# Kernel optimization log

Measured on AMD Instinct MI355X. Metric: run time of the kernel, lower is better.

## Reference

```python
import jax, jax.numpy as jnp
import numpy as np

N, H, E, R, Q = 10000, 128, 160000, 32, 1
CUT = 5.0  # cutoff_upper, cutoff_lower = 0


def setup_inputs() -> dict:
    key = jax.random.key(0)
    ks = jax.random.split(key, 16)

    def w(k, shape, fan_in):
        return jax.random.normal(k, shape, jnp.float32) / np.sqrt(fan_in).astype(np.float32)

    return dict(
        X=jax.random.normal(ks[0], (N, H, 3, 3), jnp.float32),
        charges=jax.random.normal(ks[1], (N, Q), jnp.float32),
        edge_attr=jax.random.normal(ks[2], (E, R), jnp.float32),
        edge_weight=jax.random.uniform(ks[3], (E,), jnp.float32, 0.0, CUT),
        W1=w(ks[4], (H, R + 2 * Q), R + 2 * Q), b1=jnp.zeros((H,), jnp.float32),
        W2=w(ks[5], (2 * H, H), H), b2=jnp.zeros((2 * H,), jnp.float32),
        W3=w(ks[6], (3 * H, 2 * H), 2 * H), b3=jnp.zeros((3 * H,), jnp.float32),
        Wt0=w(ks[7], (H, H), H), Wt1=w(ks[8], (H, H), H), Wt2=w(ks[9], (H, H), H),
        Wt3=w(ks[10], (H, H), H), Wt4=w(ks[11], (H, H), H), Wt5=w(ks[12], (H, H), H),
        edge_index=jax.random.randint(ks[13], (2, E), 0, N),
    )


def tensor_norm(T):
    return jnp.sum(T * T, axis=(-2, -1))  # [N, H]


def decompose(T):
    # I: mean of diagonal (scalar per channel); A: skew part; S: traceless symmetric part
    I = jnp.trace(T, axis1=-2, axis2=-1) / 3.0  # [N, H]
    Tt = jnp.swapaxes(T, -2, -1)
    A = 0.5 * (T - Tt)
    S = 0.5 * (T + Tt) - I[..., None, None] * jnp.eye(3, dtype=T.dtype)
    return I, A, S


def chlin(T, W):
    # channel-mixing linear on [N, H, 3, 3]; torch Linear: y_o = sum_h x_h W[o, h]
    return jnp.einsum('nhij,oh->noij', T, W)


def vec_to_skew(v):
    # v: [N, H, 3] -> skew-symmetric [N, H, 3, 3]
    z = jnp.zeros_like(v[..., 0])
    return jnp.stack([
        jnp.stack([z, -v[..., 2], v[..., 1]], -1),
        jnp.stack([v[..., 2], z, -v[..., 0]], -1),
        jnp.stack([-v[..., 1], v[..., 0], z], -1),
    ], -2)


def skew_to_vec(A):
    return jnp.stack([A[..., 2, 1], A[..., 0, 2], A[..., 1, 0]], -1)


def reference(X, charges, edge_attr, edge_weight, W1, b1, W2, b2, W3, b3,
              Wt0, Wt1, Wt2, Wt3, Wt4, Wt5, edge_index):
    eye = jnp.eye(3, dtype=X.dtype)
    src, dst = edge_index[0], edge_index[1]
    n = X.shape[0]

    # cosine cutoff (cutoff_lower = 0)
    C = 0.5 * (jnp.cos(jnp.pi * edge_weight / CUT) + 1.0) * (edge_weight < CUT)

    # edge scalar MLP
    x = jnp.concatenate([edge_attr, charges[src], charges[dst]], axis=-1)
    x = jax.nn.silu(x @ W1.T + b1)
    x = jax.nn.silu(x @ W2.T + b2)
    x = jax.nn.silu(x @ W3.T + b3)
    x = (x * C[:, None]).reshape(-1, 3, H)  # [E, 3, H]

    X = X / (tensor_norm(X) + 1.0)[..., None, None]
    I, A, S = decompose(X)
    I = I @ Wt0.T
    A = chlin(A, Wt1)
    S = chlin(S, Wt2)
    Y = A + S + I[..., None, None] * eye

    # message passing: gather at dst, weight by edge scalars, scatter-add to src
    Im = jax.ops.segment_sum(x[:, 0, :] * I[dst], src, num_segments=n)
    Am = jax.ops.segment_sum(x[:, 1, :, None] * skew_to_vec(A)[dst], src, num_segments=n)
    Sm = jax.ops.segment_sum(x[:, 2, :, None, None] * S[dst], src, num_segments=n)
    msg = vec_to_skew(Am) + Sm + Im[..., None, None] * eye

    # O(3) equivariance: symmetrized product
    M = jnp.matmul(msg, Y) + jnp.matmul(Y, msg)
    I, A, S = decompose(M)

    _X = A + S + I[..., None, None] * eye
    normp1 = tensor_norm(_X) + 1.0
    I = I / normp1
    A = A / normp1[..., None, None]
    S = S / normp1[..., None, None]
    I = I @ Wt3.T
    A = chlin(A, Wt4)
    S = chlin(S, Wt5)
    dX = A + S + I[..., None, None] * eye
    return X + dX + jnp.matmul(dX, dX)
```

## Files before the change

### kernel.cpp

```cpp
#include <hip/hip_runtime.h>

#define NN  10000
#define HD  128
#define EE  160000
#define RD  32
#define NH  (NN * HD)

typedef __attribute__((ext_vector_type(8))) short short8_t;
typedef __attribute__((ext_vector_type(4))) float f32x4_t;
typedef __attribute__((ext_vector_type(4))) int   int4_t;

__device__ __forceinline__ float silu_f(float z) {
    return z * __builtin_amdgcn_rcpf(1.0f + __expf(-z));
}
__device__ __forceinline__ short f2b(float v) {
    unsigned u = __float_as_uint(v);
    unsigned r = (u + 0x7FFFu + ((u >> 16) & 1u)) >> 16;
    return (short)r;
}
__device__ __forceinline__ float b2f(short s) {
    return __uint_as_float(((unsigned)(unsigned short)s) << 16);
}
__device__ __forceinline__ unsigned cvt_pk(float a, float b) {
    unsigned r;
    asm("v_cvt_pk_bf16_f32 %0, %1, %2" : "=v"(r) : "v"(a), "v"(b));
    return r;
}

__global__ __launch_bounds__(256) void k_wconv(
    const float* __restrict__ W1, const float* __restrict__ W2,
    const float* __restrict__ W3,
    const float* __restrict__ Wt0, const float* __restrict__ Wt1,
    const float* __restrict__ Wt2, const float* __restrict__ Wt3,
    const float* __restrict__ Wt4, const float* __restrict__ Wt5,
    short* __restrict__ W1b, short* __restrict__ W2b, short* __restrict__ W3b,
    short* __restrict__ WtPh, short* __restrict__ WtPl,
    short* __restrict__ WtFh, short* __restrict__ WtFl)
{
    const int i = blockIdx.x * 256 + threadIdx.x;
    if (i < 8192) {
        const int j = i & 7, lane = (i >> 3) & 63;
        const int kb = (i >> 9) & 1, ct = i >> 10;
        const int n = ct * 16 + (lane & 15);
        const int k = kb * 32 + (lane >> 4) * 8 + j;
        W1b[i] = (k < 34) ? f2b(W1[n * 34 + k]) : (short)0;
        return;
    }
    int j2 = i - 8192;
    if (j2 < 32768) {
        const int j = j2 & 7, lane = (j2 >> 3) & 63;
        const int kb = (j2 >> 9) & 3, ct = j2 >> 11;
        const int n = ct * 16 + (lane & 15);
        const int k = kb * 32 + (lane >> 4) * 8 + j;
        W2b[j2] = f2b(W2[n * 128 + k]);
        return;
    }
    j2 -= 32768;
    if (j2 < 98304) {
        const int j = j2 & 7, lane = (j2 >> 3) & 63;
        const int kb = (j2 >> 9) & 7, ct = j2 >> 12;
        const int n = ct * 16 + (lane & 15);
        const int k = kb * 32 + (lane >> 4) * 8 + j;
        W3b[j2] = f2b(W3[n * 256 + k]);
        return;
    }
    j2 -= 98304;
    if (j2 < 6 * 16384) {
        const int m = j2 >> 14, idx = j2 & 16383;
        const float* src = (m == 0) ? Wt0 : (m == 1) ? Wt1 : (m == 2) ? Wt2
                         : (m == 3) ? Wt3 : (m == 4) ? Wt4 : Wt5;
        const float w = src[idx];
        const short hi = f2b(w);
        const short lo = f2b(w - b2f(hi));
        if (m < 3) { WtPh[m * 16384 + idx] = hi; WtPl[m * 16384 + idx] = lo; }
        else       { WtFh[(m - 3) * 16384 + idx] = hi; WtFl[(m - 3) * 16384 + idx] = lo; }
    }
}

template <bool FIN, bool WB>
__global__ __launch_bounds__(512, 4) void k_mix(
    const float* __restrict__ X,
    const float* __restrict__ Yin, const float* __restrict__ MSGin,
    const short* __restrict__ Wh,  const short* __restrict__ Wl,
    float* __restrict__ outp, short* __restrict__ ybf)
{
    extern __shared__ __align__(16) char smem[];
    short* sBh = (short*)smem;
    short* sBl = sBh + 144 * 128;
    float* sC  = (float*)smem;

    const int tid = threadIdx.x;
    const int n0  = blockIdx.x * 16;

#pragma unroll 2
    for (int i = 0; i < 4; i++) {
        const int p  = i * 512 + tid;
        const int nl = p >> 7, h = p & 127;
        float dec[9];
        if constexpr (!FIN) {
            const float* t = X + ((size_t)((n0 + nl) * HD + h)) * 9;
            float T[9];
#pragma unroll
            for (int q = 0; q < 9; q++) T[q] = t[q];
            float nrm = 0.f;
#pragma unroll
            for (int q = 0; q < 9; q++) nrm = fmaf(T[q], T[q], nrm);
            const float inv = 1.0f / (nrm + 1.0f);
#pragma unroll
            for (int q = 0; q < 9; q++) T[q] *= inv;
            const float I = (T[0] + T[4] + T[8]) * (1.0f / 3.0f);
            dec[0] = I;
            dec[1] = 0.5f * (T[7] - T[5]);
            dec[2] = 0.5f * (T[2] - T[6]);
            dec[3] = 0.5f * (T[3] - T[1]);
            dec[4] = T[0] - I;
            dec[5] = 0.5f * (T[1] + T[3]);
            dec[6] = 0.5f * (T[2] + T[6]);
            dec[7] = T[4] - I;
            dec[8] = 0.5f * (T[5] + T[7]);
        } else {
            const int basep = (n0 + nl) * HD + h;
            float yv[9], mv[9];
#pragma unroll
            for (int c = 0; c < 9; c++) {
                yv[c] = Yin[(size_t)c * NH + basep];
                mv[c] = MSGin[(size_t)c * NH + basep];
            }
            float Yt[9], G[9];
            {
                const float I = yv[0], a0 = yv[1], a1 = yv[2], a2 = yv[3];
                const float s00 = yv[4], s01 = yv[5], s02 = yv[6], s11 = yv[7], s12 = yv[8];
                const float s22 = -s00 - s11;
                Yt[0] = I + s00; Yt[1] = s01 - a2; Yt[2] = s02 + a1;
                Yt[3] = s01 + a2; Yt[4] = I + s11; Yt[5] = s12 - a0;
                Yt[6] = s02 - a1; Yt[7] = s12 + a0; Yt[8] = I + s22;
            }
            {
                const float I = mv[0], a0 = mv[1], a1 = mv[2], a2 = mv[3];
                const float s00 = mv[4], s01 = mv[5], s02 = mv[6], s11 = mv[7], s12 = mv[8];
                const float s22 = -s00 - s11;
                G[0] = I + s00; G[1] = s01 - a2; G[2] = s02 + a1;
                G[3] = s01 + a2; G[4] = I + s11; G[5] = s12 - a0;
                G[6] = s02 - a1; G[7] = s12 + a0; G[8] = I + s22;
            }
            float M[9];
#pragma unroll
            for (int r = 0; r < 3; r++)
#pragma unroll
                for (int cc = 0; cc < 3; cc++) {
                    float a = 0.f;
#pragma unroll
                    for (int k = 0; k < 3; k++)
                        a += G[r * 3 + k] * Yt[k * 3 + cc]
                           + Yt[r * 3 + k] * G[k * 3 + cc];
                    M[r * 3 + cc] = a;
                }
            const float I2 = (M[0] + M[4] + M[8]) * (1.0f / 3.0f);
            const float a0 = 0.5f * (M[7] - M[5]);
            const float a1 = 0.5f * (M[2] - M[6]);
            const float a2 = 0.5f * (M[3] - M[1]);
            const float s00 = M[0] - I2, s11 = M[4] - I2;
            const float s01 = 0.5f * (M[1] + M[3]);
            const float s02 = 0.5f * (M[2] + M[6]);
            const float s12 = 0.5f * (M[5] + M[7]);
            const float s22 = -s00 - s11;
            const float nrm = 2.f * (a0 * a0 + a1 * a1 + a2 * a2)
                            + (s00 * s00 + s11 * s11 + s22 * s22)
                            + 2.f * (s01 * s01 + s02 * s02 + s12 * s12)
                            + 3.f * I2 * I2;
            const float inv = 1.0f / (nrm + 1.0f);
            dec[0] = I2 * inv;  dec[1] = a0 * inv;  dec[2] = a1 * inv;
            dec[3] = a2 * inv;  dec[4] = s00 * inv; dec[5] = s01 * inv;
            dec[6] = s02 * inv; dec[7] = s11 * inv; dec[8] = s12 * inv;
        }
        const int sw = (nl & 7) << 3;
        const int hx = h ^ sw;
#pragma unroll
        for (int c = 0; c < 9; c++) {
            const float v  = dec[c];
            const short hi = f2b(v);
            const short lo = f2b(v - b2f(hi));
            const int idx = (c * 16 + nl) * 128 + hx;
            sBh[idx] = hi;
            sBl[idx] = lo;
        }
    }
    __syncthreads();

    const int lane = tid & 63, wid = tid >> 6;
    const int l15 = lane & 15, g = lane >> 4;
    f32x4_t acc[9];
#pragma unroll
    for (int c = 0; c < 9; c++) acc[c] = {0.f, 0.f, 0.f, 0.f};

    const int bsw = (l15 & 7) << 3;
    const int o   = wid * 16 + l15;
#pragma unroll
    for (int k = 0; k < 4; k++) {
        const int k0  = k * 32 + g * 8;
        const int ksw = k0 ^ bsw;
#pragma unroll
        for (int w = 0; w < 3; w++) {
            const size_t aoff = (size_t)w * 16384 + (size_t)o * 128 + k0;
            const short8_t Ah = *(const short8_t*)(Wh + aoff);
            const short8_t Al = *(const short8_t*)(Wl + aoff);
            const int ct0 = (w == 0) ? 0 : (w == 1 ? 1 : 4);
            const int ctn = (w == 0) ? 1 : (w == 1 ? 3 : 5);
            for (int cc = 0; cc < ctn; cc++) {
                const int ct = ct0 + cc;
                const int boff = (ct * 16 + l15) * 128 + ksw;
                const short8_t Bh = *(const short8_t*)&sBh[boff];
                const short8_t Bl = *(const short8_t*)&sBl[boff];
                acc[ct] = __builtin_amdgcn_mfma_f32_16x16x32_bf16(Al, Bh, acc[ct], 0, 0, 0);
                acc[ct] = __builtin_amdgcn_mfma_f32_16x16x32_bf16(Ah, Bl, acc[ct], 0, 0, 0);
                acc[ct] = __builtin_amdgcn_mfma_f32_16x16x32_bf16(Ah, Bh, acc[ct], 0, 0, 0);
            }
        }
    }
    __syncthreads();

    const int csw = (l15 & 7) << 2;
    {
        const int o0 = wid * 16 + g * 4;
#pragma unroll
        for (int ct = 0; ct < 9; ct++)
            *(f32x4_t*)&sC[(ct * 16 + l15) * 128 + (o0 ^ csw)] = acc[ct];
    }
    __syncthreads();

    if constexpr (!FIN) {
        for (int i = tid; i < 144 * 32; i += 512) {
            const int row = i >> 5, q = i & 31;
            const int c = row >> 4, nl = row & 15;
            const int sw = (nl & 7) << 2;
            const f32x4_t v = *(const f32x4_t*)&sC[row * 128 + ((q * 4) ^ sw)];
            const size_t oo = (size_t)c * NH + (size_t)(n0 + nl) * HD + q * 4;
            *(f32x4_t*)&outp[oo] = v;
            if constexpr (WB) {
                uint2 u;
                u.x = cvt_pk(v[0], v[1]);
                u.y = cvt_pk(v[2], v[3]);
                *(uint2*)&ybf[oo] = u;
            }
        }
    } else {
#pragma unroll 2
        for (int i = 0; i < 4; i++) {
            const int p  = i * 512 + tid;
            const int nl = p >> 7, oo = p & 127;
            const int sw = (nl & 7) << 2;
            const int ox = oo ^ sw;
            float a9[9];
#pragma unroll
            for (int c = 0; c < 9; c++) a9[c] = sC[(c * 16 + nl) * 128 + ox];
            float D[9];
            {
                const float I = a9[0], a0 = a9[1], a1 = a9[2], a2 = a9[3];
                const float s00 = a9[4], s01 = a9[5], s02 = a9[6];
                const float s11 = a9[7], s12 = a9[8];
                const float s22 = -s00 - s11;
                D[0] = I + s00; D[1] = s01 - a2; D[2] = s02 + a1;
                D[3] = s01 + a2; D[4] = I + s11; D[5] = s12 - a0;
                D[6] = s02 - a1; D[7] = s12 + a0; D[8] = I + s22;
            }
            const size_t xbase = ((size_t)((n0 + nl) * HD + oo)) * 9;
            float T[9];
#pragma unroll
            for (int q = 0; q < 9; q++) T[q] = X[xbase + q];
            float nrm = 0.f;
#pragma unroll
            for (int q = 0; q < 9; q++) nrm = fmaf(T[q], T[q], nrm);
            const float inv = 1.0f / (nrm + 1.0f);
            float* op = outp + xbase;
#pragma unroll
            for (int r = 0; r < 3; r++)
#pragma unroll
                for (int cc = 0; cc < 3; cc++) {
                    float dd2 = 0.f;
#pragma unroll
                    for (int k = 0; k < 3; k++)
                        dd2 = fmaf(D[r * 3 + k], D[k * 3 + cc], dd2);
                    op[r * 3 + cc] = T[r * 3 + cc] * inv + D[r * 3 + cc] + dd2;
                }
        }
    }
}

__global__ __launch_bounds__(256) void k_count(const int* __restrict__ EI,
                                               int* __restrict__ cnt)
{
    const int e = blockIdx.x * 256 + threadIdx.x;
    atomicAdd(&cnt[EI[e]], 1);
}

__global__ __launch_bounds__(256) void k_scan(const int* __restrict__ cnt,
                                              int* __restrict__ offs,
                                              int* __restrict__ cur)
{
    __shared__ int part[256];
    const int tid = threadIdx.x;
    const int per = (NN + 255) / 256;
    int s = 0;
    for (int i = 0; i < per; i++) {
        const int idx = tid * per + i;
        if (idx < NN) s += cnt[idx];
    }
    part[tid] = s;
    __syncthreads();
    if (tid == 0) {
        int r = 0;
        for (int i = 0; i < 256; i++) { const int t = part[i]; part[i] = r; r += t; }
        offs[NN] = r;
    }
    __syncthreads();
    int run = part[tid];
    for (int i = 0; i < per; i++) {
        const int idx = tid * per + i;
        if (idx < NN) {
            offs[idx] = run;
            cur[idx]  = run;
            run += cnt[idx];
        }
    }
}

__global__ __launch_bounds__(256) void k_fill(const int* __restrict__ EI,
                                              int* __restrict__ cur,
                                              int* __restrict__ EIDS,
                                              int* __restrict__ DSTS)
{
    const int e = blockIdx.x * 256 + threadIdx.x;
    const int s = EI[e];
    const int pos = atomicAdd(&cur[s], 1);
    EIDS[pos] = e;
    DSTS[pos] = EI[EE + e];
}

__global__ __launch_bounds__(512, 4) void k_edge_mfma(
    const float* __restrict__ EA, const float* __restrict__ CH,
    const float* __restrict__ EW, const int*   __restrict__ EI,
    const short* __restrict__ W1b, const float* __restrict__ b1,
    const short* __restrict__ W2b, const float* __restrict__ b2,
    const short* __restrict__ W3b, const float* __restrict__ b3,
    short* __restrict__ XC)
{
    __shared__ __align__(16) short sH2[64 * 256];
    __shared__ __align__(16) short sH1[64 * 128];
    __shared__ float sCut[64];

    short* sIn = sH2;
    const int tid = threadIdx.x;
    const int e0  = blockIdx.x * 64;

    {
        int4_t z = {0, 0, 0, 0};
        ((int4_t*)sIn)[tid] = z;
    }
    __syncthreads();
    {
        const float4 v = ((const float4*)(EA + (size_t)e0 * RD))[tid];
        const int e = tid >> 3;
        const int k = (tid & 7) * 4;
        short4 sv;
        sv.x = f2b(v.x); sv.y = f2b(v.y); sv.z = f2b(v.z); sv.w = f2b(v.w);
        *(short4*)&sIn[e * 64 + (k ^ ((e & 7) << 3))] = sv;
        if (tid < 64) {
            const int ee = tid;
            const int s = EI[e0 + ee];
            const int d = EI[EE + e0 + ee];
            const int sw = (ee & 7) << 3;
            sIn[ee * 64 + (32 ^ sw)] = f2b(CH[s]);
            sIn[ee * 64 + (33 ^ sw)] = f2b(CH[d]);
            const float w = EW[e0 + ee];
            sCut[ee] = (w < 5.0f)
                     ? 0.5f * (__cosf(0.62831853071795864769f * w) + 1.0f) : 0.0f;
        }
    }
    __syncthreads();

    const int lane = tid & 63;
    const int wid  = tid >> 6;
    const int l15  = lane & 15;
    const int g    = lane >> 4;
    const int fsw  = l15 << 3;

    {
        short8_t E1[4][2];
#pragma unroll
        for (int at = 0; at < 4; at++) {
            const int row = at * 16 + l15;
            const int x = (row & 7) << 3;
            E1[at][0] = *(const short8_t*)&sIn[row * 64 + ((g * 8) ^ x)];
            E1[at][1] = *(const short8_t*)&sIn[row * 64 + ((32 + g * 8) ^ x)];
        }
        const int ct = wid;
        const float4 b4 = *(const float4*)&b1[ct * 16 + g * 4];
        const short8_t av0 = *(const short8_t*)(W1b + (size_t)((ct * 2 + 0) * 64 + lane) * 8);
        const short8_t av1 = *(const short8_t*)(W1b + (size_t)((ct * 2 + 1) * 64 + lane) * 8);
        const int fcol = ct * 16 + g * 4;
#pragma unroll
        for (int at = 0; at < 4; at++) {
            f32x4_t acc = {b4.x, b4.y, b4.z, b4.w};
            acc = __builtin_amdgcn_mfma_f32_16x16x32_bf16(av0, E1[at][0], acc, 0, 0, 0);
            acc = __builtin_amdgcn_mfma_f32_16x16x32_bf16(av1, E1[at][1], acc, 0, 0, 0);
            const int edge = at * 16 + l15;
            uint2 u;
            u.x = cvt_pk(silu_f(acc[0]), silu_f(acc[1]));
            u.y = cvt_pk(silu_f(acc[2]), silu_f(acc[3]));
            *(uint2*)&sH1[edge * 128 + (fcol ^ fsw)] = u;
        }
    }
    __syncthreads();

    {
        short8_t E2[4][4];
#pragma unroll
        for (int at = 0; at < 4; at++) {
            const int row = at * 16 + l15;
            const int x = (row & 15) << 3;
#pragma unroll
            for (int kb = 0; kb < 4; kb++)
                E2[at][kb] = *(const short8_t*)&sH1[row * 128 + ((kb * 32 + g * 8) ^ x)];
        }
#pragma unroll
        for (int c = 0; c < 2; c++) {
            const int ct = c * 8 + wid;
            const float4 b4 = *(const float4*)&b2[ct * 16 + g * 4];
            const int fcol = ct * 16 + g * 4;
            f32x4_t acc[4];
#pragma unroll
            for (int at = 0; at < 4; at++) acc[at] = {b4.x, b4.y, b4.z, b4.w};
#pragma unroll
            for (int kb = 0; kb < 4; kb++) {
                const short8_t av = *(const short8_t*)(W2b + (size_t)((ct * 4 + kb) * 64 + lane) * 8);
#pragma unroll
                for (int at = 0; at < 4; at++)
                    acc[at] = __builtin_amdgcn_mfma_f32_16x16x32_bf16(av, E2[at][kb], acc[at], 0, 0, 0);
            }
#pragma unroll
            for (int at = 0; at < 4; at++) {
                const int edge = at * 16 + l15;
                uint2 u;
                u.x = cvt_pk(silu_f(acc[at][0]), silu_f(acc[at][1]));
                u.y = cvt_pk(silu_f(acc[at][2]), silu_f(acc[at][3]));
                *(uint2*)&sH2[edge * 256 + (fcol ^ fsw)] = u;
            }
        }
    }
    __syncthreads();

    {
        short8_t E3[4][8];
#pragma unroll
        for (int at = 0; at < 4; at++) {
            const int row = at * 16 + l15;
            const int x = (row & 15) << 3;
#pragma unroll
            for (int kb = 0; kb < 8; kb++)
                E3[at][kb] = *(const short8_t*)&sH2[row * 256 + ((kb * 32 + g * 8) ^ x)];
        }
        float cut[4];
#pragma unroll
        for (int at = 0; at < 4; at++) cut[at] = sCut[at * 16 + l15];
        for (int c = 0; c < 3; c++) {
            const int ct = c * 8 + wid;
            const float4 b4 = *(const float4*)&b3[ct * 16 + g * 4];
            const int fcol = ct * 16 + g * 4;
            f32x4_t acc[4];
#pragma unroll
            for (int at = 0; at < 4; at++) acc[at] = {b4.x, b4.y, b4.z, b4.w};
#pragma unroll
            for (int kb = 0; kb < 8; kb++) {
                const short8_t av = *(const short8_t*)(W3b + (size_t)((ct * 8 + kb) * 64 + lane) * 8);
#pragma unroll
                for (int at = 0; at < 4; at++)
                    acc[at] = __builtin_amdgcn_mfma_f32_16x16x32_bf16(av, E3[at][kb], acc[at], 0, 0, 0);
            }
#pragma unroll
            for (int at = 0; at < 4; at++) {
                const int edge = at * 16 + l15;
                const float cv = cut[at];
                uint2 u;
                u.x = cvt_pk(silu_f(acc[at][0]) * cv, silu_f(acc[at][1]) * cv);
                u.y = cvt_pk(silu_f(acc[at][2]) * cv, silu_f(acc[at][3]) * cv);
                *(uint2*)&XC[(size_t)(e0 + edge) * 384 + fcol] = u;
            }
        }
    }
}

__global__ __launch_bounds__(256) void k_edge_atomic(
    const float* __restrict__ EA, const float* __restrict__ CH,
    const float* __restrict__ EW, const int*   __restrict__ EI,
    const float* __restrict__ W1, const float* __restrict__ b1,
    const float* __restrict__ W2, const float* __restrict__ b2,
    const float* __restrict__ W3, const float* __restrict__ b3,
    const float* __restrict__ Y,  float* __restrict__ MSG)
{
    __shared__ __align__(16) float sInf[32 * 35];
    __shared__ __align__(16) float sH1f[32 * 132];
    __shared__ __align__(16) float sH2f[32 * 260];
    __shared__ __align__(16) float sXcf[32 * 132];
    __shared__ float sCc[32];
    __shared__ int   sS[32], sD[32];

    const int e0  = blockIdx.x * 32;
    const int tid = threadIdx.x;

    {
        const float4 v = ((const float4*)(EA + (size_t)e0 * RD))[tid];
        const int e = tid >> 3;
        const int k = (tid & 7) * 4;
        float* p = sInf + e * 35 + k;
        p[0] = v.x; p[1] = v.y; p[2] = v.z; p[3] = v.w;
    }
    if (tid < 32) {
        const int e = tid;
        const int s = EI[e0 + e];
        const int d = EI[EE + e0 + e];
        sS[e] = s; sD[e] = d;
        sInf[e * 35 + 32] = CH[s];
        sInf[e * 35 + 33] = CH[d];
        const float w = EW[e0 + e];
        sCc[e] = (w < 5.0f) ? 0.5f * (__cosf(0.62831853071795864769f * w) + 1.0f)
                            : 0.0f;
    }
    __syncthreads();

    const int e  = tid & 31;
    const int og = tid >> 5;

    {
        float acc[16];
#pragma unroll
        for (int j = 0; j < 16; j++) acc[j] = b1[og * 16 + j];
        for (int k = 0; k < 34; k++) {
            const float v = sInf[e * 35 + k];
#pragma unroll
            for (int j = 0; j < 16; j++)
                acc[j] = fmaf(v, W1[(og * 16 + j) * 34 + k], acc[j]);
        }
#pragma unroll
        for (int j = 0; j < 16; j++)
            sH1f[e * 132 + og * 16 + j] = silu_f(acc[j]);
    }
    __syncthreads();

    {
        float acc[32];
#pragma unroll
        for (int j = 0; j < 32; j++) acc[j] = b2[og * 32 + j];
        for (int hq = 0; hq < 32; hq++) {
            const float4 v = *(const float4*)&sH1f[e * 132 + hq * 4];
#pragma unroll
            for (int j = 0; j < 32; j++) {
                const float4 w =
                    *(const float4*)&W2[(size_t)(og * 32 + j) * 128 + hq * 4];
                acc[j] = fmaf(v.x, w.x, fmaf(v.y, w.y,
                         fmaf(v.z, w.z, fmaf(v.w, w.w, acc[j]))));
            }
        }
#pragma unroll
        for (int j = 0; j < 32; j++)
            sH2f[e * 260 + og * 32 + j] = silu_f(acc[j]);
    }
    __syncthreads();

    for (int c = 0; c < 3; c++) {
        {
            float acc[16];
#pragma unroll
            for (int j = 0; j < 16; j++) acc[j] = b3[c * 128 + og * 16 + j];
            for (int hq = 0; hq < 64; hq++) {
                const float4 v = *(const float4*)&sH2f[e * 260 + hq * 4];
#pragma unroll
                for (int j = 0; j < 16; j++) {
                    const float4 w = *(const float4*)
                        &W3[(size_t)(c * 128 + og * 16 + j) * 256 + hq * 4];
                    acc[j] = fmaf(v.x, w.x, fmaf(v.y, w.y,
                             fmaf(v.z, w.z, fmaf(v.w, w.w, acc[j]))));
                }
            }
            const float cc = sCc[e];
#pragma unroll
            for (int j = 0; j < 16; j++)
                sXcf[e * 132 + og * 16 + j] = silu_f(acc[j]) * cc;
        }
        __syncthreads();
        {
            const int h  = tid & 127;
            const int eh = tid >> 7;
#pragma unroll 4
            for (int i = 0; i < 16; i++) {
                const int ee = (eh << 4) | i;
                const int s = sS[ee], d = sD[ee];
                const float xv = sXcf[ee * 132 + h];
                const int sb = s * HD + h, db = d * HD + h;
                if (c == 0) {
                    atomicAdd(&MSG[0 * (size_t)NH + sb], xv * Y[0 * (size_t)NH + db]);
                } else if (c == 1) {
#pragma unroll
                    for (int cc2 = 1; cc2 < 4; cc2++)
                        atomicAdd(&MSG[(size_t)cc2 * NH + sb],
                                  xv * Y[(size_t)cc2 * NH + db]);
                } else {
#pragma unroll
                    for (int cc2 = 4; cc2 < 9; cc2++)
                        atomicAdd(&MSG[(size_t)cc2 * NH + sb],
                                  xv * Y[(size_t)cc2 * NH + db]);
                }
            }
        }
        __syncthreads();
    }
}

__device__ __forceinline__ float ldy(const float* p) { return *p; }
__device__ __forceinline__ float ldy(const short* p) { return b2f(*p); }

template <typename YT>
__global__ __launch_bounds__(256) void k_gather(
    const short* __restrict__ XC, const YT* __restrict__ Y,
    const int* __restrict__ offs, const int* __restrict__ EIDS,
    const int* __restrict__ DSTS, float* __restrict__ MSG)
{
    const int tid = threadIdx.x;
    const int nl  = tid >> 7, h = tid & 127;
    const int n   = blockIdx.x * 2 + nl;
    const int beg = offs[n], end = offs[n + 1];

    float m[9];
#pragma unroll
    for (int c = 0; c < 9; c++) m[c] = 0.f;

    for (int p = beg; p < end; ++p) {
        const int eid = EIDS[p];
        const int dst = DSTS[p];
        const size_t xb = (size_t)eid * 384;
        const float x0 = b2f(XC[xb + h]);
        const float x1 = b2f(XC[xb + 128 + h]);
        const float x2 = b2f(XC[xb + 256 + h]);
        const int yb = dst * HD + h;
        m[0] = fmaf(x0, ldy(Y + 0 * (size_t)NH + yb), m[0]);
        m[1] = fmaf(x1, ldy(Y + 1 * (size_t)NH + yb), m[1]);
        m[2] = fmaf(x1, ldy(Y + 2 * (size_t)NH + yb), m[2]);
        m[3] = fmaf(x1, ldy(Y + 3 * (size_t)NH + yb), m[3]);
        m[4] = fmaf(x2, ldy(Y + 4 * (size_t)NH + yb), m[4]);
        m[5] = fmaf(x2, ldy(Y + 5 * (size_t)NH + yb), m[5]);
        m[6] = fmaf(x2, ldy(Y + 6 * (size_t)NH + yb), m[6]);
        m[7] = fmaf(x2, ldy(Y + 7 * (size_t)NH + yb), m[7]);
        m[8] = fmaf(x2, ldy(Y + 8 * (size_t)NH + yb), m[8]);
    }
    const int base = n * HD + h;
#pragma unroll
    for (int c = 0; c < 9; c++) MSG[(size_t)c * NH + base] = m[c];
}

static inline size_t align_up(size_t v, size_t a) { return (v + a - 1) & ~(a - 1); }

extern "C" void kernel_launch(void* const* d_in, const int* in_sizes, int n_in,
                              void* d_out, int out_size, void* d_ws, size_t ws_size,
                              hipStream_t stream)
{
    const float* X   = (const float*)d_in[0];
    const float* CH  = (const float*)d_in[1];
    const float* EA  = (const float*)d_in[2];
    const float* EW  = (const float*)d_in[3];
    const float* W1  = (const float*)d_in[4];
    const float* b1  = (const float*)d_in[5];
    const float* W2  = (const float*)d_in[6];
    const float* b2  = (const float*)d_in[7];
    const float* W3  = (const float*)d_in[8];
    const float* b3  = (const float*)d_in[9];
    const float* Wt0 = (const float*)d_in[10];
    const float* Wt1 = (const float*)d_in[11];
    const float* Wt2 = (const float*)d_in[12];
    const float* Wt3 = (const float*)d_in[13];
    const float* Wt4 = (const float*)d_in[14];
    const float* Wt5 = (const float*)d_in[15];
    const int*   EI  = (const int*)d_in[16];
    float* out = (float*)d_out;

    size_t off = 0;
    float* Y    = (float*)((char*)d_ws + off); off = align_up(off + (size_t)9 * NH * 4, 64);
    float* MSG  = (float*)((char*)d_ws + off); off = align_up(off + (size_t)9 * NH * 4, 64);
    int*   cnt  = (int*)((char*)d_ws + off);   off = align_up(off + (size_t)NN * 4, 64);
    int*   cur  = (int*)((char*)d_ws + off);   off = align_up(off + (size_t)NN * 4, 64);
    int*   offs = (int*)((char*)d_ws + off);   off = align_up(off + (size_t)(NN + 1) * 4, 64);
    int*   EIDS = (int*)((char*)d_ws + off);   off = align_up(off + (size_t)EE * 4, 64);
    int*   DSTS = (int*)((char*)d_ws + off);   off = align_up(off + (size_t)EE * 4, 64);
    short* W1b  = (short*)((char*)d_ws + off); off = align_up(off + (size_t)8192 * 2, 64);
    short* W2b  = (short*)((char*)d_ws + off); off = align_up(off + (size_t)32768 * 2, 64);
    short* W3b  = (short*)((char*)d_ws + off); off = align_up(off + (size_t)98304 * 2, 64);
    short* WtPh = (short*)((char*)d_ws + off); off = align_up(off + (size_t)3 * 16384 * 2, 64);
    short* WtPl = (short*)((char*)d_ws + off); off = align_up(off + (size_t)3 * 16384 * 2, 64);
    short* WtFh = (short*)((char*)d_ws + off); off = align_up(off + (size_t)3 * 16384 * 2, 64);
    short* WtFl = (short*)((char*)d_ws + off); off = align_up(off + (size_t)3 * 16384 * 2, 64);
    short* XC   = (short*)((char*)d_ws + off); off = align_up(off + (size_t)EE * 384 * 2, 64);
    const size_t need_plain = off;
    short* Ybf  = (short*)((char*)d_ws + off); off = align_up(off + (size_t)9 * NH * 2, 64);
    const size_t need_ybf = off;

    k_wconv<<<928, 256, 0, stream>>>(W1, W2, W3, Wt0, Wt1, Wt2, Wt3, Wt4, Wt5,
                                     W1b, W2b, W3b, WtPh, WtPl, WtFh, WtFl);

    if (ws_size >= need_plain) {
        const bool use_ybf = (ws_size >= need_ybf);
        if (use_ybf)
            k_mix<false, true><<<NN / 16, 512, 73728, stream>>>(
                X, Y, Y, WtPh, WtPl, Y, Ybf);
        else
            k_mix<false, false><<<NN / 16, 512, 73728, stream>>>(
                X, Y, Y, WtPh, WtPl, Y, nullptr);

        hipMemsetAsync(cnt, 0, (size_t)NN * sizeof(int), stream);
        k_count<<<EE / 256, 256, 0, stream>>>(EI, cnt);
        k_scan<<<1, 256, 0, stream>>>(cnt, offs, cur);
        k_fill<<<EE / 256, 256, 0, stream>>>(EI, cur, EIDS, DSTS);
        k_edge_mfma<<<EE / 64, 512, 0, stream>>>(EA, CH, EW, EI,
                                                 W1b, b1, W2b, b2, W3b, b3, XC);
        if (use_ybf)
            k_gather<short><<<NN / 2, 256, 0, stream>>>(XC, Ybf, offs, EIDS, DSTS, MSG);
        else
            k_gather<float><<<NN / 2, 256, 0, stream>>>(XC, Y, offs, EIDS, DSTS, MSG);
    } else {
        k_mix<false, false><<<NN / 16, 512, 73728, stream>>>(
            X, Y, Y, WtPh, WtPl, Y, nullptr);
        hipMemsetAsync(MSG, 0, (size_t)9 * NH * sizeof(float), stream);
        k_edge_atomic<<<EE / 32, 256, 0, stream>>>(EA, CH, EW, EI,
                                                   W1, b1, W2, b2, W3, b3, Y, MSG);
    }

    k_mix<true, false><<<NN / 16, 512, 73728, stream>>>(X, Y, MSG, WtFh, WtFl, out, nullptr);
}
```

Measured before the change: 306.3 us.

## Fuse neighbor gather into final mix kernel and write edge filters in CSR order

The separate gather kernel is removed. The final mixing kernel now accumulates messages directly from CSR-ordered edge filters and the bf16 Y, so the fp32 MSG buffer no longer makes a global round trip. The edge MLP kernel reads edges through the sorted permutation (EIDS), so its XC output is stored in CSR order and the gather reads contiguous rows. The prep kernel also stops writing fp32 Y on the fast path. The trade-off is that the fused gather runs inside a 512-thread, high-LDS kernel with 16 nodes per block, which may reduce parallelism for the irregular gather loop. Reads of edge attributes inside the MLP kernel also become scattered.

```diff
diff --git a/kernel.cpp b/kernel.cpp
--- a/kernel.cpp
+++ b/kernel.cpp
@@ -77,12 +77,12 @@
     }
 }
 
-template <bool FIN, bool WB>
-__global__ __launch_bounds__(512, 4) void k_mix(
+
+template <bool YBF16>
+__global__ __launch_bounds__(512, 4) void k_mix_prep(
     const float* __restrict__ X,
-    const float* __restrict__ Yin, const float* __restrict__ MSGin,
-    const short* __restrict__ Wh,  const short* __restrict__ Wl,
-    float* __restrict__ outp, short* __restrict__ ybf)
+    const short* __restrict__ Wh, const short* __restrict__ Wl,
+    float* __restrict__ Yf, short* __restrict__ ybf)
 {
     extern __shared__ __align__(16) char smem[];
     short* sBh = (short*)smem;
@@ -96,83 +96,27 @@
     for (int i = 0; i < 4; i++) {
         const int p  = i * 512 + tid;
         const int nl = p >> 7, h = p & 127;
+        const float* t = X + ((size_t)((n0 + nl) * HD + h)) * 9;
+        float T[9];
+#pragma unroll
+        for (int q = 0; q < 9; q++) T[q] = t[q];
+        float nrm = 0.f;
+#pragma unroll
+        for (int q = 0; q < 9; q++) nrm = fmaf(T[q], T[q], nrm);
+        const float inv = 1.0f / (nrm + 1.0f);
+#pragma unroll
+        for (int q = 0; q < 9; q++) T[q] *= inv;
+        const float I = (T[0] + T[4] + T[8]) * (1.0f / 3.0f);
         float dec[9];
-        if constexpr (!FIN) {
-            const float* t = X + ((size_t)((n0 + nl) * HD + h)) * 9;
-            float T[9];
-#pragma unroll
-            for (int q = 0; q < 9; q++) T[q] = t[q];
-            float nrm = 0.f;
-#pragma unroll
-            for (int q = 0; q < 9; q++) nrm = fmaf(T[q], T[q], nrm);
-            const float inv = 1.0f / (nrm + 1.0f);
-#pragma unroll
-            for (int q = 0; q < 9; q++) T[q] *= inv;
-            const float I = (T[0] + T[4] + T[8]) * (1.0f / 3.0f);
-            dec[0] = I;
-            dec[1] = 0.5f * (T[7] - T[5]);
-            dec[2] = 0.5f * (T[2] - T[6]);
-            dec[3] = 0.5f * (T[3] - T[1]);
-            dec[4] = T[0] - I;
-            dec[5] = 0.5f * (T[1] + T[3]);
-            dec[6] = 0.5f * (T[2] + T[6]);
-            dec[7] = T[4] - I;
-            dec[8] = 0.5f * (T[5] + T[7]);
-        } else {
-            const int basep = (n0 + nl) * HD + h;
-            float yv[9], mv[9];
-#pragma unroll
-            for (int c = 0; c < 9; c++) {
-                yv[c] = Yin[(size_t)c * NH + basep];
-                mv[c] = MSGin[(size_t)c * NH + basep];
-            }
-            float Yt[9], G[9];
-            {
-                const float I = yv[0], a0 = yv[1], a1 = yv[2], a2 = yv[3];
-                const float s00 = yv[4], s01 = yv[5], s02 = yv[6], s11 = yv[7], s12 = yv[8];
-                const float s22 = -s00 - s11;
-                Yt[0] = I + s00; Yt[1] = s01 - a2; Yt[2] = s02 + a1;
-                Yt[3] = s01 + a2; Yt[4] = I + s11; Yt[5] = s12 - a0;
-                Yt[6] = s02 - a1; Yt[7] = s12 + a0; Yt[8] = I + s22;
-            }
-            {
-                const float I = mv[0], a0 = mv[1], a1 = mv[2], a2 = mv[3];
-                const float s00 = mv[4], s01 = mv[5], s02 = mv[6], s11 = mv[7], s12 = mv[8];
-                const float s22 = -s00 - s11;
-                G[0] = I + s00; G[1] = s01 - a2; G[2] = s02 + a1;
-                G[3] = s01 + a2; G[4] = I + s11; G[5] = s12 - a0;
-                G[6] = s02 - a1; G[7] = s12 + a0; G[8] = I + s22;
-            }
-            float M[9];
-#pragma unroll
-            for (int r = 0; r < 3; r++)
-#pragma unroll
-                for (int cc = 0; cc < 3; cc++) {
-                    float a = 0.f;
-#pragma unroll
-                    for (int k = 0; k < 3; k++)
-                        a += G[r * 3 + k] * Yt[k * 3 + cc]
-                           + Yt[r * 3 + k] * G[k * 3 + cc];
-                    M[r * 3 + cc] = a;
-                }
-            const float I2 = (M[0] + M[4] + M[8]) * (1.0f / 3.0f);
-            const float a0 = 0.5f * (M[7] - M[5]);
-            const float a1 = 0.5f * (M[2] - M[6]);
-            const float a2 = 0.5f * (M[3] - M[1]);
-            const float s00 = M[0] - I2, s11 = M[4] - I2;
-            const float s01 = 0.5f * (M[1] + M[3]);
-            const float s02 = 0.5f * (M[2] + M[6]);
-            const float s12 = 0.5f * (M[5] + M[7]);
-            const float s22 = -s00 - s11;
-            const float nrm = 2.f * (a0 * a0 + a1 * a1 + a2 * a2)
-                            + (s00 * s00 + s11 * s11 + s22 * s22)
-                            + 2.f * (s01 * s01 + s02 * s02 + s12 * s12)
-                            + 3.f * I2 * I2;
-            const float inv = 1.0f / (nrm + 1.0f);
-            dec[0] = I2 * inv;  dec[1] = a0 * inv;  dec[2] = a1 * inv;
-            dec[3] = a2 * inv;  dec[4] = s00 * inv; dec[5] = s01 * inv;
-            dec[6] = s02 * inv; dec[7] = s11 * inv; dec[8] = s12 * inv;
-        }
+        dec[0] = I;
+        dec[1] = 0.5f * (T[7] - T[5]);
+        dec[2] = 0.5f * (T[2] - T[6]);
+        dec[3] = 0.5f * (T[3] - T[1]);
+        dec[4] = T[0] - I;
+        dec[5] = 0.5f * (T[1] + T[3]);
+        dec[6] = 0.5f * (T[2] + T[6]);
+        dec[7] = T[4] - I;
+        dec[8] = 0.5f * (T[5] + T[7]);
         const int sw = (nl & 7) << 3;
         const int hx = h ^ sw;
 #pragma unroll
@@ -228,61 +172,217 @@
     }
     __syncthreads();
 
-    if constexpr (!FIN) {
-        for (int i = tid; i < 144 * 32; i += 512) {
-            const int row = i >> 5, q = i & 31;
-            const int c = row >> 4, nl = row & 15;
-            const int sw = (nl & 7) << 2;
-            const f32x4_t v = *(const f32x4_t*)&sC[row * 128 + ((q * 4) ^ sw)];
-            const size_t oo = (size_t)c * NH + (size_t)(n0 + nl) * HD + q * 4;
-            *(f32x4_t*)&outp[oo] = v;
-            if constexpr (WB) {
-                uint2 u;
-                u.x = cvt_pk(v[0], v[1]);
-                u.y = cvt_pk(v[2], v[3]);
-                *(uint2*)&ybf[oo] = u;
-            }
-        }
-    } else {
+    for (int i = tid; i < 144 * 32; i += 512) {
+        const int row = i >> 5, q = i & 31;
+        const int c = row >> 4, nl = row & 15;
+        const int sw = (nl & 7) << 2;
+        const f32x4_t v = *(const f32x4_t*)&sC[row * 128 + ((q * 4) ^ sw)];
+        const size_t oo = (size_t)c * NH + (size_t)(n0 + nl) * HD + q * 4;
+        if constexpr (YBF16) {
+            uint2 u;
+            u.x = cvt_pk(v[0], v[1]);
+            u.y = cvt_pk(v[2], v[3]);
+            *(uint2*)&ybf[oo] = u;
+        } else {
+            *(f32x4_t*)&Yf[oo] = v;
+        }
+    }
+}
+
+template <bool FUSED>
+__global__ __launch_bounds__(512, 4) void k_mix_fin(
+    const float* __restrict__ X,
+    const float* __restrict__ Yf,  const float* __restrict__ MSGf,
+    const short* __restrict__ Ybf, const short* __restrict__ XC,
+    const int* __restrict__ offs,  const int* __restrict__ DSTS,
+    const short* __restrict__ Wh,  const short* __restrict__ Wl,
+    float* __restrict__ outp)
+{
+    extern __shared__ __align__(16) char smem[];
+    short* sBh = (short*)smem;
+    short* sBl = sBh + 144 * 128;
+    float* sC  = (float*)smem;
+
+    const int tid = threadIdx.x;
+    const int n0  = blockIdx.x * 16;
+
+    for (int i = 0; i < 4; i++) {
+        const int p  = i * 512 + tid;
+        const int nl = p >> 7, h = p & 127;
+        const int basep = (n0 + nl) * HD + h;
+        float yv[9], mv[9];
+        if constexpr (FUSED) {
+            const int n = n0 + nl;
+            const int beg = offs[n], end = offs[n + 1];
+#pragma unroll
+            for (int c = 0; c < 9; c++) mv[c] = 0.f;
+            for (int pp = beg; pp < end; ++pp) {
+                const int dst = DSTS[pp];
+                const size_t xb = (size_t)pp * 384;
+                const float x0 = b2f(XC[xb + h]);
+                const float x1 = b2f(XC[xb + 128 + h]);
+                const float x2 = b2f(XC[xb + 256 + h]);
+                const int yb = dst * HD + h;
+                mv[0] = fmaf(x0, b2f(Ybf[0 * (size_t)NH + yb]), mv[0]);
+                mv[1] = fmaf(x1, b2f(Ybf[1 * (size_t)NH + yb]), mv[1]);
+                mv[2] = fmaf(x1, b2f(Ybf[2 * (size_t)NH + yb]), mv[2]);
+                mv[3] = fmaf(x1, b2f(Ybf[3 * (size_t)NH + yb]), mv[3]);
+                mv[4] = fmaf(x2, b2f(Ybf[4 * (size_t)NH + yb]), mv[4]);
+                mv[5] = fmaf(x2, b2f(Ybf[5 * (size_t)NH + yb]), mv[5]);
+                mv[6] = fmaf(x2, b2f(Ybf[6 * (size_t)NH + yb]), mv[6]);
+                mv[7] = fmaf(x2, b2f(Ybf[7 * (size_t)NH + yb]), mv[7]);
+                mv[8] = fmaf(x2, b2f(Ybf[8 * (size_t)NH + yb]), mv[8]);
+            }
+#pragma unroll
+            for (int c = 0; c < 9; c++) yv[c] = b2f(Ybf[(size_t)c * NH + basep]);
+        } else {
+#pragma unroll
+            for (int c = 0; c < 9; c++) {
+                yv[c] = Yf[(size_t)c * NH + basep];
+                mv[c] = MSGf[(size_t)c * NH + basep];
+            }
+        }
+        float Yt[9], G[9];
+        {
+            const float I = yv[0], a0 = yv[1], a1 = yv[2], a2 = yv[3];
+            const float s00 = yv[4], s01 = yv[5], s02 = yv[6], s11 = yv[7], s12 = yv[8];
+            const float s22 = -s00 - s11;
+            Yt[0] = I + s00; Yt[1] = s01 - a2; Yt[2] = s02 + a1;
+            Yt[3] = s01 + a2; Yt[4] = I + s11; Yt[5] = s12 - a0;
+            Yt[6] = s02 - a1; Yt[7] = s12 + a0; Yt[8] = I + s22;
+        }
+        {
+            const float I = mv[0], a0 = mv[1], a1 = mv[2], a2 = mv[3];
+            const float s00 = mv[4], s01 = mv[5], s02 = mv[6], s11 = mv[7], s12 = mv[8];
+            const float s22 = -s00 - s11;
+            G[0] = I + s00; G[1] = s01 - a2; G[2] = s02 + a1;
+            G[3] = s01 + a2; G[4] = I + s11; G[5] = s12 - a0;
+            G[6] = s02 - a1; G[7] = s12 + a0; G[8] = I + s22;
+        }
+        float M[9];
+#pragma unroll
+        for (int r = 0; r < 3; r++)
+#pragma unroll
+            for (int cc = 0; cc < 3; cc++) {
+                float a = 0.f;
+#pragma unroll
+                for (int k = 0; k < 3; k++)
+                    a += G[r * 3 + k] * Yt[k * 3 + cc]
+                       + Yt[r * 3 + k] * G[k * 3 + cc];
+                M[r * 3 + cc] = a;
+            }
+        const float I2 = (M[0] + M[4] + M[8]) * (1.0f / 3.0f);
+        const float a0 = 0.5f * (M[7] - M[5]);
+        const float a1 = 0.5f * (M[2] - M[6]);
+        const float a2 = 0.5f * (M[3] - M[1]);
+        const float s00 = M[0] - I2, s11 = M[4] - I2;
+        const float s01 = 0.5f * (M[1] + M[3]);
+        const float s02 = 0.5f * (M[2] + M[6]);
+        const float s12 = 0.5f * (M[5] + M[7]);
+        const float s22 = -s00 - s11;
+        const float nrm = 2.f * (a0 * a0 + a1 * a1 + a2 * a2)
+                        + (s00 * s00 + s11 * s11 + s22 * s22)
+                        + 2.f * (s01 * s01 + s02 * s02 + s12 * s12)
+                        + 3.f * I2 * I2;
+        const float inv = 1.0f / (nrm + 1.0f);
+        float dec[9];
+        dec[0] = I2 * inv;  dec[1] = a0 * inv;  dec[2] = a1 * inv;
+        dec[3] = a2 * inv;  dec[4] = s00 * inv; dec[5] = s01 * inv;
+        dec[6] = s02 * inv; dec[7] = s11 * inv; dec[8] = s12 * inv;
+
+        const int sw = (nl & 7) << 3;
+        const int hx = h ^ sw;
+#pragma unroll
+        for (int c = 0; c < 9; c++) {
+            const float v  = dec[c];
+            const short hi = f2b(v);
+            const short lo = f2b(v - b2f(hi));
+            const int idx = (c * 16 + nl) * 128 + hx;
+            sBh[idx] = hi;
+            sBl[idx] = lo;
+        }
+    }
+    __syncthreads();
+
+    const int lane = tid & 63, wid = tid >> 6;
+    const int l15 = lane & 15, g = lane >> 4;
+    f32x4_t acc[9];
+#pragma unroll
+    for (int c = 0; c < 9; c++) acc[c] = {0.f, 0.f, 0.f, 0.f};
+
+    const int bsw = (l15 & 7) << 3;
+    const int o   = wid * 16 + l15;
+#pragma unroll
+    for (int k = 0; k < 4; k++) {
+        const int k0  = k * 32 + g * 8;
+        const int ksw = k0 ^ bsw;
+#pragma unroll
+        for (int w = 0; w < 3; w++) {
+            const size_t aoff = (size_t)w * 16384 + (size_t)o * 128 + k0;
+            const short8_t Ah = *(const short8_t*)(Wh + aoff);
+            const short8_t Al = *(const short8_t*)(Wl + aoff);
+            const int ct0 = (w == 0) ? 0 : (w == 1 ? 1 : 4);
+            const int ctn = (w == 0) ? 1 : (w == 1 ? 3 : 5);
+            for (int cc = 0; cc < ctn; cc++) {
+                const int ct = ct0 + cc;
+                const int boff = (ct * 16 + l15) * 128 + ksw;
+                const short8_t Bh = *(const short8_t*)&sBh[boff];
+                const short8_t Bl = *(const short8_t*)&sBl[boff];
+                acc[ct] = __builtin_amdgcn_mfma_f32_16x16x32_bf16(Al, Bh, acc[ct], 0, 0, 0);
+                acc[ct] = __builtin_amdgcn_mfma_f32_16x16x32_bf16(Ah, Bl, acc[ct], 0, 0, 0);
+                acc[ct] = __builtin_amdgcn_mfma_f32_16x16x32_bf16(Ah, Bh, acc[ct], 0, 0, 0);
+            }
+        }
+    }
+    __syncthreads();
+
+    const int csw = (l15 & 7) << 2;
+    {
+        const int o0 = wid * 16 + g * 4;
+#pragma unroll
+        for (int ct = 0; ct < 9; ct++)
+            *(f32x4_t*)&sC[(ct * 16 + l15) * 128 + (o0 ^ csw)] = acc[ct];
+    }
+    __syncthreads();
+
 #pragma unroll 2
-        for (int i = 0; i < 4; i++) {
-            const int p  = i * 512 + tid;
-            const int nl = p >> 7, oo = p & 127;
-            const int sw = (nl & 7) << 2;
-            const int ox = oo ^ sw;
-            float a9[9];
-#pragma unroll
-            for (int c = 0; c < 9; c++) a9[c] = sC[(c * 16 + nl) * 128 + ox];
-            float D[9];
-            {
-                const float I = a9[0], a0 = a9[1], a1 = a9[2], a2 = a9[3];
-                const float s00 = a9[4], s01 = a9[5], s02 = a9[6];
-                const float s11 = a9[7], s12 = a9[8];
-                const float s22 = -s00 - s11;
-                D[0] = I + s00; D[1] = s01 - a2; D[2] = s02 + a1;
-                D[3] = s01 + a2; D[4] = I + s11; D[5] = s12 - a0;
-                D[6] = s02 - a1; D[7] = s12 + a0; D[8] = I + s22;
-            }
-            const size_t xbase = ((size_t)((n0 + nl) * HD + oo)) * 9;
-            float T[9];
-#pragma unroll
-            for (int q = 0; q < 9; q++) T[q] = X[xbase + q];
-            float nrm = 0.f;
-#pragma unroll
-            for (int q = 0; q < 9; q++) nrm = fmaf(T[q], T[q], nrm);
-            const float inv = 1.0f / (nrm + 1.0f);
-            float* op = outp + xbase;
-#pragma unroll
-            for (int r = 0; r < 3; r++)
-#pragma unroll
-                for (int cc = 0; cc < 3; cc++) {
-                    float dd2 = 0.f;
-#pragma unroll
-                    for (int k = 0; k < 3; k++)
-                        dd2 = fmaf(D[r * 3 + k], D[k * 3 + cc], dd2);
-                    op[r * 3 + cc] = T[r * 3 + cc] * inv + D[r * 3 + cc] + dd2;
-                }
-        }
+    for (int i = 0; i < 4; i++) {
+        const int p  = i * 512 + tid;
+        const int nl = p >> 7, oo = p & 127;
+        const int sw = (nl & 7) << 2;
+        const int ox = oo ^ sw;
+        float a9[9];
+#pragma unroll
+        for (int c = 0; c < 9; c++) a9[c] = sC[(c * 16 + nl) * 128 + ox];
+        float D[9];
+        {
+            const float I = a9[0], a0 = a9[1], a1 = a9[2], a2 = a9[3];
+            const float s00 = a9[4], s01 = a9[5], s02 = a9[6];
+            const float s11 = a9[7], s12 = a9[8];
+            const float s22 = -s00 - s11;
+            D[0] = I + s00; D[1] = s01 - a2; D[2] = s02 + a1;
+            D[3] = s01 + a2; D[4] = I + s11; D[5] = s12 - a0;
+            D[6] = s02 - a1; D[7] = s12 + a0; D[8] = I + s22;
+        }
+        const size_t xbase = ((size_t)((n0 + nl) * HD + oo)) * 9;
+        float T[9];
+#pragma unroll
+        for (int q = 0; q < 9; q++) T[q] = X[xbase + q];
+        float nrm = 0.f;
+#pragma unroll
+        for (int q = 0; q < 9; q++) nrm = fmaf(T[q], T[q], nrm);
+        const float inv = 1.0f / (nrm + 1.0f);
+        float* op = outp + xbase;
+#pragma unroll
+        for (int r = 0; r < 3; r++)
+#pragma unroll
+            for (int cc = 0; cc < 3; cc++) {
+                float dd2 = 0.f;
+#pragma unroll
+                for (int k = 0; k < 3; k++)
+                    dd2 = fmaf(D[r * 3 + k], D[k * 3 + cc], dd2);
+                op[r * 3 + cc] = T[r * 3 + cc] * inv + D[r * 3 + cc] + dd2;
+            }
     }
 }
 
@@ -339,6 +439,7 @@
 __global__ __launch_bounds__(512, 4) void k_edge_mfma(
     const float* __restrict__ EA, const float* __restrict__ CH,
     const float* __restrict__ EW, const int*   __restrict__ EI,
+    const int*   __restrict__ EIDS,
     const short* __restrict__ W1b, const float* __restrict__ b1,
     const short* __restrict__ W2b, const float* __restrict__ b2,
     const short* __restrict__ W3b, const float* __restrict__ b3,
@@ -347,6 +448,7 @@
     __shared__ __align__(16) short sH2[64 * 256];
     __shared__ __align__(16) short sH1[64 * 128];
     __shared__ float sCut[64];
+    __shared__ int   sEid[64];
 
     short* sIn = sH2;
     const int tid = threadIdx.x;
@@ -355,24 +457,27 @@
     {
         int4_t z = {0, 0, 0, 0};
         ((int4_t*)sIn)[tid] = z;
-    }
-    __syncthreads();
-    {
-        const float4 v = ((const float4*)(EA + (size_t)e0 * RD))[tid];
-        const int e = tid >> 3;
+        if (tid < 64) sEid[tid] = EIDS[e0 + tid];
+    }
+    __syncthreads();
+    {
+        const int ee  = tid >> 3;
+        const int eid = sEid[ee];
+        const float4 v = *(const float4*)(EA + (size_t)eid * RD + (tid & 7) * 4);
         const int k = (tid & 7) * 4;
         short4 sv;
         sv.x = f2b(v.x); sv.y = f2b(v.y); sv.z = f2b(v.z); sv.w = f2b(v.w);
-        *(short4*)&sIn[e * 64 + (k ^ ((e & 7) << 3))] = sv;
+        *(short4*)&sIn[ee * 64 + (k ^ ((ee & 7) << 3))] = sv;
         if (tid < 64) {
-            const int ee = tid;
-            const int s = EI[e0 + ee];
-            const int d = EI[EE + e0 + ee];
-            const int sw = (ee & 7) << 3;
-            sIn[ee * 64 + (32 ^ sw)] = f2b(CH[s]);
-            sIn[ee * 64 + (33 ^ sw)] = f2b(CH[d]);
-            const float w = EW[e0 + ee];
-            sCut[ee] = (w < 5.0f)
+            const int e2  = tid;
+            const int eid2 = sEid[e2];
+            const int s = EI[eid2];
+            const int d = EI[EE + eid2];
+            const int sw = (e2 & 7) << 3;
+            sIn[e2 * 64 + (32 ^ sw)] = f2b(CH[s]);
+            sIn[e2 * 64 + (33 ^ sw)] = f2b(CH[d]);
+            const float w = EW[eid2];
+            sCut[e2] = (w < 5.0f)
                      ? 0.5f * (__cosf(0.62831853071795864769f * w) + 1.0f) : 0.0f;
         }
     }
@@ -613,47 +718,6 @@
         }
         __syncthreads();
     }
-}
-
-__device__ __forceinline__ float ldy(const float* p) { return *p; }
-__device__ __forceinline__ float ldy(const short* p) { return b2f(*p); }
-
-template <typename YT>
-__global__ __launch_bounds__(256) void k_gather(
-    const short* __restrict__ XC, const YT* __restrict__ Y,
-    const int* __restrict__ offs, const int* __restrict__ EIDS,
-    const int* __restrict__ DSTS, float* __restrict__ MSG)
-{
-    const int tid = threadIdx.x;
-    const int nl  = tid >> 7, h = tid & 127;
-    const int n   = blockIdx.x * 2 + nl;
-    const int beg = offs[n], end = offs[n + 1];
-
-    float m[9];
-#pragma unroll
-    for (int c = 0; c < 9; c++) m[c] = 0.f;
-
-    for (int p = beg; p < end; ++p) {
-        const int eid = EIDS[p];
-        const int dst = DSTS[p];
-        const size_t xb = (size_t)eid * 384;
-        const float x0 = b2f(XC[xb + h]);
-        const float x1 = b2f(XC[xb + 128 + h]);
-        const float x2 = b2f(XC[xb + 256 + h]);
-        const int yb = dst * HD + h;
-        m[0] = fmaf(x0, ldy(Y + 0 * (size_t)NH + yb), m[0]);
-        m[1] = fmaf(x1, ldy(Y + 1 * (size_t)NH + yb), m[1]);
-        m[2] = fmaf(x1, ldy(Y + 2 * (size_t)NH + yb), m[2]);
-        m[3] = fmaf(x1, ldy(Y + 3 * (size_t)NH + yb), m[3]);
-        m[4] = fmaf(x2, ldy(Y + 4 * (size_t)NH + yb), m[4]);
-        m[5] = fmaf(x2, ldy(Y + 5 * (size_t)NH + yb), m[5]);
-        m[6] = fmaf(x2, ldy(Y + 6 * (size_t)NH + yb), m[6]);
-        m[7] = fmaf(x2, ldy(Y + 7 * (size_t)NH + yb), m[7]);
-        m[8] = fmaf(x2, ldy(Y + 8 * (size_t)NH + yb), m[8]);
-    }
-    const int base = n * HD + h;
-#pragma unroll
-    for (int c = 0; c < 9; c++) MSG[(size_t)c * NH + base] = m[c];
 }
 
 static inline size_t align_up(size_t v, size_t a) { return (v + a - 1) & ~(a - 1); }
@@ -697,39 +761,29 @@
     short* WtFh = (short*)((char*)d_ws + off); off = align_up(off + (size_t)3 * 16384 * 2, 64);
     short* WtFl = (short*)((char*)d_ws + off); off = align_up(off + (size_t)3 * 16384 * 2, 64);
     short* XC   = (short*)((char*)d_ws + off); off = align_up(off + (size_t)EE * 384 * 2, 64);
-    const size_t need_plain = off;
     short* Ybf  = (short*)((char*)d_ws + off); off = align_up(off + (size_t)9 * NH * 2, 64);
-    const size_t need_ybf = off;
+    const size_t need_fast = off;
 
     k_wconv<<<928, 256, 0, stream>>>(W1, W2, W3, Wt0, Wt1, Wt2, Wt3, Wt4, Wt5,
                                      W1b, W2b, W3b, WtPh, WtPl, WtFh, WtFl);
 
-    if (ws_size >= need_plain) {
-        const bool use_ybf = (ws_size >= need_ybf);
-        if (use_ybf)
-            k_mix<false, true><<<NN / 16, 512, 73728, stream>>>(
-                X, Y, Y, WtPh, WtPl, Y, Ybf);
-        else
-            k_mix<false, false><<<NN / 16, 512, 73728, stream>>>(
-                X, Y, Y, WtPh, WtPl, Y, nullptr);
+    if (ws_size >= need_fast) {
+        k_mix_prep<true><<<NN / 16, 512, 73728, stream>>>(X, WtPh, WtPl, Y, Ybf);
 
         hipMemsetAsync(cnt, 0, (size_t)NN * sizeof(int), stream);
         k_count<<<EE / 256, 256, 0, stream>>>(EI, cnt);
         k_scan<<<1, 256, 0, stream>>>(cnt, offs, cur);
         k_fill<<<EE / 256, 256, 0, stream>>>(EI, cur, EIDS, DSTS);
-        k_edge_mfma<<<EE / 64, 512, 0, stream>>>(EA, CH, EW, EI,
+        k_edge_mfma<<<EE / 64, 512, 0, stream>>>(EA, CH, EW, EI, EIDS,
                                                  W1b, b1, W2b, b2, W3b, b3, XC);
-        if (use_ybf)
-            k_gather<short><<<NN / 2, 256, 0, stream>>>(XC, Ybf, offs, EIDS, DSTS, MSG);
-        else
-            k_gather<float><<<NN / 2, 256, 0, stream>>>(XC, Y, offs, EIDS, DSTS, MSG);
+        k_mix_fin<true><<<NN / 16, 512, 73728, stream>>>(
+            X, Y, MSG, Ybf, XC, offs, DSTS, WtFh, WtFl, out);
     } else {
-        k_mix<false, false><<<NN / 16, 512, 73728, stream>>>(
-            X, Y, Y, WtPh, WtPl, Y, nullptr);
+        k_mix_prep<false><<<NN / 16, 512, 73728, stream>>>(X, WtPh, WtPl, Y, Ybf);
         hipMemsetAsync(MSG, 0, (size_t)9 * NH * sizeof(float), stream);
         k_edge_atomic<<<EE / 32, 256, 0, stream>>>(EA, CH, EW, EI,
                                                    W1, b1, W2, b2, W3, b3, Y, MSG);
-    }
-
-    k_mix<true, false><<<NN / 16, 512, 73728, stream>>>(X, Y, MSG, WtFh, WtFl, out, nullptr);
-}
+        k_mix_fin<false><<<NN / 16, 512, 73728, stream>>>(
+            X, Y, MSG, Ybf, XC, offs, DSTS, WtFh, WtFl, out);
+    }
+}
```

New measurement: 346.9 us. 1.13x slower.
